# Optimization experiments

Measured on AMD Instinct MI355X. Metric: run time of the kernel, lower is better.

## Reference

```python
import jax, jax.numpy as jnp
import numpy as np

B = 32768      # rows
L = 512        # sequence_length
H = 1024       # inter_layer_size
E = 128        # encoding_size
K = 8          # number of (shifting_type, transformer_ID) combinations / decoders


def setup_inputs() -> dict:
    key = jax.random.key(0)
    ks = jax.random.split(key, 8)
    feats = jax.random.normal(ks[0], (B, L), jnp.float32)
    ids = jax.random.randint(ks[1], (B,), 0, K).astype(jnp.float32)
    x = jnp.concatenate([feats, ids[:, None]], axis=1)  # [B, L+1], last col = combination ID

    def init_w(k, shape, fan_in):
        return jax.random.normal(k, shape, jnp.float32) / np.float32(np.sqrt(fan_in))

    # shared encoder: Linear(L->H), Linear(H->E)  (weights stored [in, out])
    We1 = init_w(ks[2], (L, H), L); be1 = jnp.zeros((H,), jnp.float32)
    We2 = init_w(ks[3], (H, E), H); be2 = jnp.zeros((E,), jnp.float32)
    # per-ID decoders stacked along expert dim K: Linear(E->H), Linear(H->L)
    Wd1 = init_w(ks[4], (K, E, H), E); bd1 = jnp.zeros((K, H), jnp.float32)
    Wd2 = init_w(ks[5], (K, H, L), H); bd2 = jnp.zeros((K, L), jnp.float32)
    return dict(x=x, We1=We1, be1=be1, We2=We2, be2=be2,
                Wd1=Wd1, bd1=bd1, Wd2=Wd2, bd2=bd2)


def reference(x, We1, be1, We2, be2, Wd1, bd1, Wd2, bd2):
    seq_len = We1.shape[0]
    n_experts = Wd1.shape[0]
    ids = x[:, seq_len].astype(jnp.int32)          # routing column
    # torch code emits rows grouped by unique ID (torch.unique returns sorted ids);
    # jnp.argsort is stable, so within-group original order is preserved.
    order = jnp.argsort(ids)
    xs = x[order, :seq_len]                        # [B, L] grouped features
    ids_s = ids[order]                             # [B]

    # shared encoder MLP (LeakyReLU slope 0.01, torch default)
    h = jax.nn.leaky_relu(xs @ We1 + be1)          # [B, H]
    z = jax.nn.leaky_relu(h @ We2 + be2)           # [B, E]

    # dense expert dispatch: run every decoder, select per-row expert via one-hot
    hd = jax.nn.leaky_relu(jnp.einsum('be,keh->kbh', z, Wd1) + bd1[:, None, :])  # [K, B, H]
    y_all = jnp.einsum('kbh,khl->kbl', hd, Wd2) + bd2[:, None, :]                # [K, B, L]
    onehot = (ids_s[None, :] == jnp.arange(n_experts)[:, None]).astype(y_all.dtype)  # [K, B]
    return jnp.einsum('kb,kbl->bl', onehot, y_all)  # [B, L]
```

## Files before the change

### kernel.cpp

```cpp
#include <hip/hip_runtime.h>
#include <hip/hip_bf16.h>

#define B_ROWS 32768
#define L_DIM 512
#define H_DIM 1024
#define E_DIM 128
#define K_EXP 8
#define NBLK 128

typedef __bf16 bf16x8 __attribute__((ext_vector_type(8)));
typedef float f32x4 __attribute__((ext_vector_type(4)));

__device__ __forceinline__ void gload16(const void* src, void* dst) {
    __builtin_amdgcn_global_load_lds(
        (const __attribute__((address_space(1))) unsigned int*)src,
        (__attribute__((address_space(3))) unsigned int*)dst, 16, 0, 0);
}

__global__ void k_ids_hist(const float* __restrict__ x, int* __restrict__ ids,
                           int* __restrict__ hist) {
    __shared__ int lh[K_EXP];
    int t = threadIdx.x;
    if (t < K_EXP) lh[t] = 0;
    __syncthreads();
    int i = blockIdx.x * 256 + t;
    int id = (int)x[(size_t)i * (L_DIM + 1) + L_DIM];
    ids[i] = id;
    atomicAdd(&lh[id], 1);
    __syncthreads();
    if (t < K_EXP) hist[blockIdx.x * K_EXP + t] = lh[t];
}

__global__ void k_scan(const int* __restrict__ hist, int* __restrict__ base,
                       int* __restrict__ seg, int* __restrict__ tp) {
    __shared__ int c[K_EXP];
    __shared__ int sseg[K_EXP + 1];
    int k = threadIdx.x;
    if (k < K_EXP) {
        int run = 0;
        for (int b = 0; b < NBLK; ++b) {
            base[b * K_EXP + k] = run;
            run += hist[b * K_EXP + k];
        }
        c[k] = run;
    }
    __syncthreads();
    if (k == 0) {
        int s = 0, t2 = 0;
        for (int e = 0; e < K_EXP; ++e) {
            sseg[e] = s; seg[e] = s; tp[e] = t2;
            s += c[e]; t2 += (c[e] + 127) >> 7;
        }
        sseg[K_EXP] = s; seg[K_EXP] = s; tp[K_EXP] = t2;
    }
    __syncthreads();
    if (k < K_EXP) {
        int s0 = sseg[k];
        for (int b = 0; b < NBLK; ++b) base[b * K_EXP + k] += s0;
    }
}

__global__ void k_order(const int* __restrict__ ids, const int* __restrict__ base,
                        int* __restrict__ order) {
    __shared__ int sid[256];
    int t = threadIdx.x;
    int i = blockIdx.x * 256 + t;
    int my = ids[i];
    sid[t] = my;
    __syncthreads();
    int rank = 0;
    for (int j = 0; j < t; ++j) rank += (sid[j] == my) ? 1 : 0;
    order[base[blockIdx.x * K_EXP + my] + rank] = i;
}

__global__ void k_gather(const float* __restrict__ x, const int* __restrict__ order,
                         __hip_bfloat16* __restrict__ xs) {
    int idx = blockIdx.x * 256 + threadIdx.x;
    int p = idx >> 7;
    int c4 = (idx & 127) << 2;
    int src = order[p];
    const float* sp = x + (size_t)src * (L_DIM + 1) + c4;
    __hip_bfloat16 v[4];
    v[0] = __float2bfloat16(sp[0]);
    v[1] = __float2bfloat16(sp[1]);
    v[2] = __float2bfloat16(sp[2]);
    v[3] = __float2bfloat16(sp[3]);
    *(uint2*)(xs + (size_t)p * L_DIM + c4) = *(uint2*)v;
}

__global__ void k_transpose(const float* __restrict__ W, __hip_bfloat16* __restrict__ Wt,
                            int KDim, int NDim) {
    __shared__ float tile[32][33];
    int k0 = blockIdx.x << 5, n0 = blockIdx.y << 5;
    const float* Wb = W + (size_t)blockIdx.z * KDim * NDim;
    __hip_bfloat16* Wtb = Wt + (size_t)blockIdx.z * KDim * NDim;
    int tx = threadIdx.x & 31, ty = threadIdx.x >> 5;
    for (int i = ty; i < 32; i += 8)
        tile[i][tx] = Wb[(size_t)(k0 + i) * NDim + n0 + tx];
    __syncthreads();
    for (int i = ty; i < 32; i += 8)
        Wtb[(size_t)(n0 + i) * KDim + k0 + tx] = __float2bfloat16(tile[tx][i]);
}

template <int BM, int KD, int ND, bool GROUPED, bool LEAKY, bool OUT_BF16>
__launch_bounds__(256)
__global__ void gemm_u(const __hip_bfloat16* __restrict__ A,
                       const __hip_bfloat16* __restrict__ Bt,
                       const float* __restrict__ bias,
                       void* __restrict__ Cout,
                       const int* __restrict__ seg, const int* __restrict__ tp) {
    static_assert(!GROUPED || BM == 128, "grouped tiles are 128 rows");
    constexpr int NNT = ND / 128;
    constexpr int NMT = GROUPED ? (B_ROWS / 128 + K_EXP) : (B_ROWS / BM);
    constexpr int TOT = NMT * NNT;
    static_assert(TOT % 8 == 0, "XCD chunking needs TOT % 8 == 0");
    constexpr int ACH = BM * 32;
    constexpr int SLOT = ACH + 128 * 32;
    constexpr int NK = KD / 32;
    constexpr int VG = (BM == 128) ? 4 : 3;

    __shared__ __align__(16) __hip_bfloat16 smem[3 * SLOT];
    const int id = blockIdx.x;
    const int wg = (id & 7) * (TOT / 8) + (id >> 3);
    const int mt = wg / NNT, nt = wg % NNT;
    const int n0 = nt << 7;
    int m0, mEnd;
    const __hip_bfloat16* Bp = Bt;
    const float* bp = bias;
    if (GROUPED) {
        if (mt >= tp[K_EXP]) return;
        int e = 0;
        while (mt >= tp[e + 1]) ++e;
        m0 = seg[e] + ((mt - tp[e]) << 7);
        mEnd = seg[e + 1];
        Bp += (size_t)e * KD * ND;
        bp += (size_t)e * ND;
    } else {
        m0 = mt * BM;
        mEnd = m0 + BM;
    }
    const int t = threadIdx.x, w = t >> 6, l = t & 63;
    constexpr int FM = BM / 32;
    const int wm = w >> 1, wn = w & 1, g = l >> 4, li = l & 15;
    const int r0 = l >> 2, s0 = l & 3;

    f32x4 acc[FM][4];
#pragma unroll
    for (int i = 0; i < FM; ++i)
#pragma unroll
        for (int j = 0; j < 4; ++j) acc[i][j] = (f32x4){0.f, 0.f, 0.f, 0.f};

    auto stage = [&](int b, int kt) {
#pragma unroll
        for (int qi = 0; qi < BM / 64; ++qi) {
            int q = (BM / 64) * w + qi;
            int r = q * 16 + r0;
            int ksg = s0 ^ ((r >> 1) & 3);
            int rowg = m0 + r;
            if (GROUPED) rowg = min(rowg, B_ROWS - 1);
            gload16(A + (size_t)rowg * KD + kt * 32 + ksg * 8,
                    &smem[b * SLOT + q * 512]);
        }
#pragma unroll
        for (int qi = 0; qi < 2; ++qi) {
            int q = 2 * w + qi;
            int r = q * 16 + r0;
            int ksg = s0 ^ ((r >> 1) & 3);
            gload16(Bp + (size_t)(n0 + r) * KD + kt * 32 + ksg * 8,
                    &smem[b * SLOT + ACH + q * 512]);
        }
    };

    stage(0, 0);
    stage(1, 1);
    int b = 0;
    for (int kt = 0; kt < NK; ++kt) {
        if (kt == NK - 1)
            asm volatile("s_waitcnt vmcnt(0)\ns_barrier" ::: "memory");
        else if constexpr (VG == 4)
            asm volatile("s_waitcnt vmcnt(4)\ns_barrier" ::: "memory");
        else
            asm volatile("s_waitcnt vmcnt(3)\ns_barrier" ::: "memory");
        __builtin_amdgcn_sched_barrier(0);
        if (kt + 2 < NK) stage((b + 2 >= 3) ? b - 1 : b + 2, kt + 2);
        bf16x8 af[FM], bfr[4];
#pragma unroll
        for (int fm = 0; fm < FM; ++fm) {
            int rr = wm * (FM * 16) + fm * 16 + li;
            int ss = g ^ ((rr >> 1) & 3);
            af[fm] = *(const bf16x8*)&smem[b * SLOT + rr * 32 + ss * 8];
        }
#pragma unroll
        for (int fn = 0; fn < 4; ++fn) {
            int cc = wn * 64 + fn * 16 + li;
            int ss = g ^ ((cc >> 1) & 3);
            bfr[fn] = *(const bf16x8*)&smem[b * SLOT + ACH + cc * 32 + ss * 8];
        }
        __builtin_amdgcn_s_setprio(1);
#pragma unroll
        for (int fm = 0; fm < FM; ++fm)
#pragma unroll
            for (int fn = 0; fn < 4; ++fn)
                acc[fm][fn] = __builtin_amdgcn_mfma_f32_16x16x32_bf16(
                    af[fm], bfr[fn], acc[fm][fn], 0, 0, 0);
        __builtin_amdgcn_s_setprio(0);
        b = (b + 1 >= 3) ? 0 : b + 1;
    }

    float bv[4];
#pragma unroll
    for (int fn = 0; fn < 4; ++fn) bv[fn] = bp[n0 + wn * 64 + fn * 16 + li];
#pragma unroll
    for (int fm = 0; fm < FM; ++fm)
#pragma unroll
        for (int i = 0; i < 4; ++i) {
            int r = m0 + wm * (FM * 16) + fm * 16 + g * 4 + i;
            if (!GROUPED || r < mEnd) {
#pragma unroll
                for (int fn = 0; fn < 4; ++fn) {
                    float v = acc[fm][fn][i] + bv[fn];
                    if (LEAKY) v = v > 0.f ? v : 0.01f * v;
                    size_t off = (size_t)r * ND + n0 + wn * 64 + fn * 16 + li;
                    if (OUT_BF16)
                        ((__hip_bfloat16*)Cout)[off] = __float2bfloat16(v);
                    else
                        ((float*)Cout)[off] = v;
                }
            }
        }
}

extern "C" void kernel_launch(void* const* d_in, const int* in_sizes, int n_in,
                              void* d_out, int out_size, void* d_ws, size_t ws_size,
                              hipStream_t stream) {
    (void)in_sizes; (void)n_in; (void)out_size; (void)ws_size;
    const float* x   = (const float*)d_in[0];
    const float* We1 = (const float*)d_in[1];
    const float* be1 = (const float*)d_in[2];
    const float* We2 = (const float*)d_in[3];
    const float* be2 = (const float*)d_in[4];
    const float* Wd1 = (const float*)d_in[5];
    const float* bd1 = (const float*)d_in[6];
    const float* Wd2 = (const float*)d_in[7];
    const float* bd2 = (const float*)d_in[8];
    float* out = (float*)d_out;

    char* w = (char*)d_ws;
    auto alloc = [&](size_t bytes) {
        char* p = w;
        w += (bytes + 255) & ~(size_t)255;
        return p;
    };
    int* ids   = (int*)alloc((size_t)B_ROWS * 4);
    int* order = (int*)alloc((size_t)B_ROWS * 4);
    int* hist  = (int*)alloc((size_t)NBLK * K_EXP * 4);
    int* base  = (int*)alloc((size_t)NBLK * K_EXP * 4);
    int* seg   = (int*)alloc((K_EXP + 1) * 4);
    int* tp    = (int*)alloc((K_EXP + 1) * 4);
    __hip_bfloat16* xs   = (__hip_bfloat16*)alloc((size_t)B_ROWS * L_DIM * 2);
    __hip_bfloat16* hbuf = (__hip_bfloat16*)alloc((size_t)B_ROWS * H_DIM * 2);
    __hip_bfloat16* zbuf = (__hip_bfloat16*)alloc((size_t)B_ROWS * E_DIM * 2);
    __hip_bfloat16* Wt1  = (__hip_bfloat16*)alloc((size_t)L_DIM * H_DIM * 2);
    __hip_bfloat16* Wt2  = (__hip_bfloat16*)alloc((size_t)H_DIM * E_DIM * 2);
    __hip_bfloat16* Wd1t = (__hip_bfloat16*)alloc((size_t)K_EXP * E_DIM * H_DIM * 2);
    __hip_bfloat16* Wd2t = (__hip_bfloat16*)alloc((size_t)K_EXP * H_DIM * L_DIM * 2);

    k_ids_hist<<<NBLK, 256, 0, stream>>>(x, ids, hist);
    k_scan<<<1, 64, 0, stream>>>(hist, base, seg, tp);
    k_order<<<NBLK, 256, 0, stream>>>(ids, base, order);
    k_gather<<<(B_ROWS * (L_DIM / 4)) / 256, 256, 0, stream>>>(x, order, xs);

    k_transpose<<<dim3(L_DIM / 32, H_DIM / 32, 1), 256, 0, stream>>>(We1, Wt1, L_DIM, H_DIM);
    k_transpose<<<dim3(H_DIM / 32, E_DIM / 32, 1), 256, 0, stream>>>(We2, Wt2, H_DIM, E_DIM);
    k_transpose<<<dim3(E_DIM / 32, H_DIM / 32, K_EXP), 256, 0, stream>>>(Wd1, Wd1t, E_DIM, H_DIM);
    k_transpose<<<dim3(H_DIM / 32, L_DIM / 32, K_EXP), 256, 0, stream>>>(Wd2, Wd2t, H_DIM, L_DIM);

    gemm_u<128, L_DIM, H_DIM, false, true, true>
        <<<(B_ROWS / 128) * (H_DIM / 128), 256, 0, stream>>>(xs, Wt1, be1, hbuf, nullptr, nullptr);
    gemm_u<64, H_DIM, E_DIM, false, true, true>
        <<<(B_ROWS / 64) * (E_DIM / 128), 256, 0, stream>>>(hbuf, Wt2, be2, zbuf, nullptr, nullptr);
    gemm_u<128, E_DIM, H_DIM, true, true, true>
        <<<(B_ROWS / 128 + K_EXP) * (H_DIM / 128), 256, 0, stream>>>(zbuf, Wd1t, bd1, hbuf, seg, tp);
    gemm_u<128, H_DIM, L_DIM, true, false, false>
        <<<(B_ROWS / 128 + K_EXP) * (L_DIM / 128), 256, 0, stream>>>(hbuf, Wd2t, bd2, out, seg, tp);
}
```

Baseline: 208.6 us.

## Pad expert segments to 128-row tiles and use 128x256 GEMM tiles

Rows are now scattered into a padded layout where each expert segment starts on a 128-row boundary. That removes the per-row bounds checks and the min-clamping on A loads, and lets the padded buffer run the whole encoder and decoder chain. The first-layer and decoder GEMMs move to a wider 128x256 tile, with each wave computing 128x64 and launch bounds set for two blocks per CU. The final GEMM maps padded rows back to their sorted output positions. Padding adds up to 1024 extra rows of computation, and the larger per-wave accumulator raises register pressure.

```diff
diff --git a/kernel.cpp b/kernel.cpp
--- a/kernel.cpp
+++ b/kernel.cpp
@@ -7,6 +7,8 @@
 #define E_DIM 128
 #define K_EXP 8
 #define NBLK 128
+#define MAXT 264
+#define MAXB (MAXT * 128)
 
 typedef __bf16 bf16x8 __attribute__((ext_vector_type(8)));
 typedef float f32x4 __attribute__((ext_vector_type(4)));
@@ -16,6 +18,12 @@
         (const __attribute__((address_space(1))) unsigned int*)src,
         (__attribute__((address_space(3))) unsigned int*)dst, 16, 0, 0);
 }
+
+#define M_NT 0
+#define M_SEG 1
+#define M_SEGP 10
+#define M_CNT 19
+#define M_TEXP 27
 
 __global__ void k_ids_hist(const float* __restrict__ x, int* __restrict__ ids,
                            int* __restrict__ hist) {
@@ -32,9 +40,10 @@
 }
 
 __global__ void k_scan(const int* __restrict__ hist, int* __restrict__ base,
-                       int* __restrict__ seg, int* __restrict__ tp) {
+                       int* __restrict__ meta, int* __restrict__ order_pad) {
     __shared__ int c[K_EXP];
-    __shared__ int sseg[K_EXP + 1];
+    __shared__ int sp[K_EXP + 1];
+    __shared__ int scnt[K_EXP];
     int k = threadIdx.x;
     if (k < K_EXP) {
         int run = 0;
@@ -46,18 +55,36 @@
     }
     __syncthreads();
     if (k == 0) {
-        int s = 0, t2 = 0;
+        int s = 0, p = 0;
         for (int e = 0; e < K_EXP; ++e) {
-            sseg[e] = s; seg[e] = s; tp[e] = t2;
-            s += c[e]; t2 += (c[e] + 127) >> 7;
-        }
-        sseg[K_EXP] = s; seg[K_EXP] = s; tp[K_EXP] = t2;
+            meta[M_SEG + e] = s;
+            meta[M_SEGP + e] = p;
+            meta[M_CNT + e] = c[e];
+            sp[e] = p;
+            scnt[e] = c[e];
+            s += c[e];
+            p += ((c[e] + 127) >> 7) << 7;
+        }
+        meta[M_SEG + K_EXP] = s;
+        meta[M_SEGP + K_EXP] = p;
+        sp[K_EXP] = p;
+        int nT = p >> 7;
+        meta[M_NT] = nT;
+        for (int e = 0; e < K_EXP; ++e)
+            for (int t2 = sp[e] >> 7; t2 < sp[e + 1] >> 7; ++t2)
+                meta[M_TEXP + t2] = e;
+        for (int t2 = nT; t2 < MAXT; ++t2) meta[M_TEXP + t2] = 0;
     }
     __syncthreads();
     if (k < K_EXP) {
-        int s0 = sseg[k];
+        int s0 = sp[k];
         for (int b = 0; b < NBLK; ++b) base[b * K_EXP + k] += s0;
     }
+    for (int e = 0; e < K_EXP; ++e) {
+        int st = sp[e] + scnt[e], en = sp[e + 1];
+        for (int p2 = st + k; p2 < en; p2 += 64) order_pad[p2] = 0;
+    }
+    for (int p2 = sp[K_EXP] + k; p2 < MAXB; p2 += 64) order_pad[p2] = 0;
 }
 
 __global__ void k_order(const int* __restrict__ ids, const int* __restrict__ base,
@@ -102,72 +129,59 @@
         Wtb[(size_t)(n0 + i) * KDim + k0 + tx] = __float2bfloat16(tile[tx][i]);
 }
 
-template <int BM, int KD, int ND, bool GROUPED, bool LEAKY, bool OUT_BF16>
-__launch_bounds__(256)
-__global__ void gemm_u(const __hip_bfloat16* __restrict__ A,
+template <int KD, int ND, bool GROUPED, bool LEAKY, bool OUT_BF16, bool MAPROW>
+__launch_bounds__(256, 2)
+__global__ void gemm_w(const __hip_bfloat16* __restrict__ A,
                        const __hip_bfloat16* __restrict__ Bt,
                        const float* __restrict__ bias,
                        void* __restrict__ Cout,
-                       const int* __restrict__ seg, const int* __restrict__ tp) {
-    static_assert(!GROUPED || BM == 128, "grouped tiles are 128 rows");
-    constexpr int NNT = ND / 128;
-    constexpr int NMT = GROUPED ? (B_ROWS / 128 + K_EXP) : (B_ROWS / BM);
-    constexpr int TOT = NMT * NNT;
+                       const int* __restrict__ meta) {
+    constexpr int NNT = ND / 256;
+    constexpr int TOT = MAXT * NNT;
     static_assert(TOT % 8 == 0, "XCD chunking needs TOT % 8 == 0");
-    constexpr int ACH = BM * 32;
-    constexpr int SLOT = ACH + 128 * 32;
+    constexpr int ASZ = 128 * 32;
+    constexpr int SLOT = ASZ + 256 * 32;
     constexpr int NK = KD / 32;
-    constexpr int VG = (BM == 128) ? 4 : 3;
 
     __shared__ __align__(16) __hip_bfloat16 smem[3 * SLOT];
     const int id = blockIdx.x;
     const int wg = (id & 7) * (TOT / 8) + (id >> 3);
     const int mt = wg / NNT, nt = wg % NNT;
-    const int n0 = nt << 7;
-    int m0, mEnd;
+    const int m0 = mt << 7, n0 = nt << 8;
     const __hip_bfloat16* Bp = Bt;
     const float* bp = bias;
+    int e = 0;
     if (GROUPED) {
-        if (mt >= tp[K_EXP]) return;
-        int e = 0;
-        while (mt >= tp[e + 1]) ++e;
-        m0 = seg[e] + ((mt - tp[e]) << 7);
-        mEnd = seg[e + 1];
+        e = meta[M_TEXP + mt];
         Bp += (size_t)e * KD * ND;
         bp += (size_t)e * ND;
-    } else {
-        m0 = mt * BM;
-        mEnd = m0 + BM;
     }
     const int t = threadIdx.x, w = t >> 6, l = t & 63;
-    constexpr int FM = BM / 32;
-    const int wm = w >> 1, wn = w & 1, g = l >> 4, li = l & 15;
+    const int g = l >> 4, li = l & 15;
     const int r0 = l >> 2, s0 = l & 3;
 
-    f32x4 acc[FM][4];
-#pragma unroll
-    for (int i = 0; i < FM; ++i)
+    f32x4 acc[8][4];
+#pragma unroll
+    for (int i = 0; i < 8; ++i)
 #pragma unroll
         for (int j = 0; j < 4; ++j) acc[i][j] = (f32x4){0.f, 0.f, 0.f, 0.f};
 
     auto stage = [&](int b, int kt) {
-#pragma unroll
-        for (int qi = 0; qi < BM / 64; ++qi) {
-            int q = (BM / 64) * w + qi;
-            int r = q * 16 + r0;
-            int ksg = s0 ^ ((r >> 1) & 3);
-            int rowg = m0 + r;
-            if (GROUPED) rowg = min(rowg, B_ROWS - 1);
-            gload16(A + (size_t)rowg * KD + kt * 32 + ksg * 8,
-                    &smem[b * SLOT + q * 512]);
-        }
 #pragma unroll
         for (int qi = 0; qi < 2; ++qi) {
             int q = 2 * w + qi;
             int r = q * 16 + r0;
             int ksg = s0 ^ ((r >> 1) & 3);
+            gload16(A + (size_t)(m0 + r) * KD + kt * 32 + ksg * 8,
+                    &smem[b * SLOT + q * 512]);
+        }
+#pragma unroll
+        for (int qi = 0; qi < 4; ++qi) {
+            int q = 4 * w + qi;
+            int r = q * 16 + r0;
+            int ksg = s0 ^ ((r >> 1) & 3);
             gload16(Bp + (size_t)(n0 + r) * KD + kt * 32 + ksg * 8,
-                    &smem[b * SLOT + ACH + q * 512]);
+                    &smem[b * SLOT + ASZ + q * 512]);
         }
     };
 
@@ -177,28 +191,26 @@
     for (int kt = 0; kt < NK; ++kt) {
         if (kt == NK - 1)
             asm volatile("s_waitcnt vmcnt(0)\ns_barrier" ::: "memory");
-        else if constexpr (VG == 4)
-            asm volatile("s_waitcnt vmcnt(4)\ns_barrier" ::: "memory");
         else
-            asm volatile("s_waitcnt vmcnt(3)\ns_barrier" ::: "memory");
+            asm volatile("s_waitcnt vmcnt(6)\ns_barrier" ::: "memory");
         __builtin_amdgcn_sched_barrier(0);
         if (kt + 2 < NK) stage((b + 2 >= 3) ? b - 1 : b + 2, kt + 2);
-        bf16x8 af[FM], bfr[4];
-#pragma unroll
-        for (int fm = 0; fm < FM; ++fm) {
-            int rr = wm * (FM * 16) + fm * 16 + li;
+        bf16x8 af[8], bfr[4];
+#pragma unroll
+        for (int fm = 0; fm < 8; ++fm) {
+            int rr = fm * 16 + li;
             int ss = g ^ ((rr >> 1) & 3);
             af[fm] = *(const bf16x8*)&smem[b * SLOT + rr * 32 + ss * 8];
         }
 #pragma unroll
         for (int fn = 0; fn < 4; ++fn) {
-            int cc = wn * 64 + fn * 16 + li;
+            int cc = w * 64 + fn * 16 + li;
             int ss = g ^ ((cc >> 1) & 3);
-            bfr[fn] = *(const bf16x8*)&smem[b * SLOT + ACH + cc * 32 + ss * 8];
+            bfr[fn] = *(const bf16x8*)&smem[b * SLOT + ASZ + cc * 32 + ss * 8];
         }
         __builtin_amdgcn_s_setprio(1);
 #pragma unroll
-        for (int fm = 0; fm < FM; ++fm)
+        for (int fm = 0; fm < 8; ++fm)
 #pragma unroll
             for (int fn = 0; fn < 4; ++fn)
                 acc[fm][fn] = __builtin_amdgcn_mfma_f32_16x16x32_bf16(
@@ -209,23 +221,126 @@
 
     float bv[4];
 #pragma unroll
-    for (int fn = 0; fn < 4; ++fn) bv[fn] = bp[n0 + wn * 64 + fn * 16 + li];
-#pragma unroll
-    for (int fm = 0; fm < FM; ++fm)
+    for (int fn = 0; fn < 4; ++fn) bv[fn] = bp[n0 + w * 64 + fn * 16 + li];
+    int se = 0, sp2 = 0, ce = 0;
+    if (MAPROW) { se = meta[M_SEG + e]; sp2 = meta[M_SEGP + e]; ce = meta[M_CNT + e]; }
+#pragma unroll
+    for (int fm = 0; fm < 8; ++fm)
 #pragma unroll
         for (int i = 0; i < 4; ++i) {
-            int r = m0 + wm * (FM * 16) + fm * 16 + g * 4 + i;
-            if (!GROUPED || r < mEnd) {
-#pragma unroll
-                for (int fn = 0; fn < 4; ++fn) {
-                    float v = acc[fm][fn][i] + bv[fn];
-                    if (LEAKY) v = v > 0.f ? v : 0.01f * v;
-                    size_t off = (size_t)r * ND + n0 + wn * 64 + fn * 16 + li;
-                    if (OUT_BF16)
-                        ((__hip_bfloat16*)Cout)[off] = __float2bfloat16(v);
-                    else
-                        ((float*)Cout)[off] = v;
+            int rp = m0 + fm * 16 + g * 4 + i;
+#pragma unroll
+            for (int fn = 0; fn < 4; ++fn) {
+                float v = acc[fm][fn][i] + bv[fn];
+                if (LEAKY) v = v > 0.f ? v : 0.01f * v;
+                int col = n0 + w * 64 + fn * 16 + li;
+                if (MAPROW) {
+                    int local = rp - sp2;
+                    if (local < ce)
+                        ((float*)Cout)[(size_t)(se + local) * ND + col] = v;
+                } else if (OUT_BF16) {
+                    ((__hip_bfloat16*)Cout)[(size_t)rp * ND + col] = __float2bfloat16(v);
+                } else {
+                    ((float*)Cout)[(size_t)rp * ND + col] = v;
                 }
+            }
+        }
+}
+
+template <int KD, int ND, bool LEAKY>
+__launch_bounds__(256)
+__global__ void gemm_u64(const __hip_bfloat16* __restrict__ A,
+                         const __hip_bfloat16* __restrict__ Bt,
+                         const float* __restrict__ bias,
+                         __hip_bfloat16* __restrict__ Cout) {
+    constexpr int BM = 64;
+    constexpr int NNT = ND / 128;
+    constexpr int NMT = MAXB / BM;
+    constexpr int TOT = NMT * NNT;
+    static_assert(TOT % 8 == 0, "XCD chunking needs TOT % 8 == 0");
+    constexpr int ACH = BM * 32;
+    constexpr int SLOT = ACH + 128 * 32;
+    constexpr int NK = KD / 32;
+
+    __shared__ __align__(16) __hip_bfloat16 smem[3 * SLOT];
+    const int id = blockIdx.x;
+    const int wg = (id & 7) * (TOT / 8) + (id >> 3);
+    const int mt = wg / NNT, nt = wg % NNT;
+    const int n0 = nt << 7;
+    const int m0 = mt * BM;
+    const int t = threadIdx.x, w = t >> 6, l = t & 63;
+    const int wm = w >> 1, wn = w & 1, g = l >> 4, li = l & 15;
+    const int r0 = l >> 2, s0 = l & 3;
+
+    f32x4 acc[2][4];
+#pragma unroll
+    for (int i = 0; i < 2; ++i)
+#pragma unroll
+        for (int j = 0; j < 4; ++j) acc[i][j] = (f32x4){0.f, 0.f, 0.f, 0.f};
+
+    auto stage = [&](int b, int kt) {
+        {
+            int q = w, r = q * 16 + r0;
+            int ksg = s0 ^ ((r >> 1) & 3);
+            gload16(A + (size_t)(m0 + r) * KD + kt * 32 + ksg * 8,
+                    &smem[b * SLOT + q * 512]);
+        }
+#pragma unroll
+        for (int qi = 0; qi < 2; ++qi) {
+            int q = 2 * w + qi, r = q * 16 + r0;
+            int ksg = s0 ^ ((r >> 1) & 3);
+            gload16(Bt + (size_t)(n0 + r) * KD + kt * 32 + ksg * 8,
+                    &smem[b * SLOT + ACH + q * 512]);
+        }
+    };
+
+    stage(0, 0);
+    stage(1, 1);
+    int b = 0;
+    for (int kt = 0; kt < NK; ++kt) {
+        if (kt == NK - 1)
+            asm volatile("s_waitcnt vmcnt(0)\ns_barrier" ::: "memory");
+        else
+            asm volatile("s_waitcnt vmcnt(3)\ns_barrier" ::: "memory");
+        __builtin_amdgcn_sched_barrier(0);
+        if (kt + 2 < NK) stage((b + 2 >= 3) ? b - 1 : b + 2, kt + 2);
+        bf16x8 af[2], bfr[4];
+#pragma unroll
+        for (int fm = 0; fm < 2; ++fm) {
+            int rr = wm * 32 + fm * 16 + li;
+            int ss = g ^ ((rr >> 1) & 3);
+            af[fm] = *(const bf16x8*)&smem[b * SLOT + rr * 32 + ss * 8];
+        }
+#pragma unroll
+        for (int fn = 0; fn < 4; ++fn) {
+            int cc = wn * 64 + fn * 16 + li;
+            int ss = g ^ ((cc >> 1) & 3);
+            bfr[fn] = *(const bf16x8*)&smem[b * SLOT + ACH + cc * 32 + ss * 8];
+        }
+        __builtin_amdgcn_s_setprio(1);
+#pragma unroll
+        for (int fm = 0; fm < 2; ++fm)
+#pragma unroll
+            for (int fn = 0; fn < 4; ++fn)
+                acc[fm][fn] = __builtin_amdgcn_mfma_f32_16x16x32_bf16(
+                    af[fm], bfr[fn], acc[fm][fn], 0, 0, 0);
+        __builtin_amdgcn_s_setprio(0);
+        b = (b + 1 >= 3) ? 0 : b + 1;
+    }
+
+    float bv[4];
+#pragma unroll
+    for (int fn = 0; fn < 4; ++fn) bv[fn] = bias[n0 + wn * 64 + fn * 16 + li];
+#pragma unroll
+    for (int fm = 0; fm < 2; ++fm)
+#pragma unroll
+        for (int i = 0; i < 4; ++i) {
+            int r = m0 + wm * 32 + fm * 16 + g * 4 + i;
+#pragma unroll
+            for (int fn = 0; fn < 4; ++fn) {
+                float v = acc[fm][fn][i] + bv[fn];
+                if (LEAKY) v = v > 0.f ? v : 0.01f * v;
+                Cout[(size_t)r * ND + n0 + wn * 64 + fn * 16 + li] = __float2bfloat16(v);
             }
         }
 }
@@ -251,36 +366,35 @@
         w += (bytes + 255) & ~(size_t)255;
         return p;
     };
-    int* ids   = (int*)alloc((size_t)B_ROWS * 4);
-    int* order = (int*)alloc((size_t)B_ROWS * 4);
-    int* hist  = (int*)alloc((size_t)NBLK * K_EXP * 4);
-    int* base  = (int*)alloc((size_t)NBLK * K_EXP * 4);
-    int* seg   = (int*)alloc((K_EXP + 1) * 4);
-    int* tp    = (int*)alloc((K_EXP + 1) * 4);
-    __hip_bfloat16* xs   = (__hip_bfloat16*)alloc((size_t)B_ROWS * L_DIM * 2);
-    __hip_bfloat16* hbuf = (__hip_bfloat16*)alloc((size_t)B_ROWS * H_DIM * 2);
-    __hip_bfloat16* zbuf = (__hip_bfloat16*)alloc((size_t)B_ROWS * E_DIM * 2);
+    int* ids       = (int*)alloc((size_t)B_ROWS * 4);
+    int* order_pad = (int*)alloc((size_t)MAXB * 4);
+    int* hist      = (int*)alloc((size_t)NBLK * K_EXP * 4);
+    int* base      = (int*)alloc((size_t)NBLK * K_EXP * 4);
+    int* meta      = (int*)alloc((size_t)(M_TEXP + MAXT) * 4);
+    __hip_bfloat16* xs   = (__hip_bfloat16*)alloc((size_t)MAXB * L_DIM * 2);
+    __hip_bfloat16* hbuf = (__hip_bfloat16*)alloc((size_t)MAXB * H_DIM * 2);
+    __hip_bfloat16* zbuf = (__hip_bfloat16*)alloc((size_t)MAXB * E_DIM * 2);
     __hip_bfloat16* Wt1  = (__hip_bfloat16*)alloc((size_t)L_DIM * H_DIM * 2);
     __hip_bfloat16* Wt2  = (__hip_bfloat16*)alloc((size_t)H_DIM * E_DIM * 2);
     __hip_bfloat16* Wd1t = (__hip_bfloat16*)alloc((size_t)K_EXP * E_DIM * H_DIM * 2);
     __hip_bfloat16* Wd2t = (__hip_bfloat16*)alloc((size_t)K_EXP * H_DIM * L_DIM * 2);
 
     k_ids_hist<<<NBLK, 256, 0, stream>>>(x, ids, hist);
-    k_scan<<<1, 64, 0, stream>>>(hist, base, seg, tp);
-    k_order<<<NBLK, 256, 0, stream>>>(ids, base, order);
-    k_gather<<<(B_ROWS * (L_DIM / 4)) / 256, 256, 0, stream>>>(x, order, xs);
+    k_scan<<<1, 64, 0, stream>>>(hist, base, meta, order_pad);
+    k_order<<<NBLK, 256, 0, stream>>>(ids, base, order_pad);
+    k_gather<<<(MAXB * (L_DIM / 4)) / 256, 256, 0, stream>>>(x, order_pad, xs);
 
     k_transpose<<<dim3(L_DIM / 32, H_DIM / 32, 1), 256, 0, stream>>>(We1, Wt1, L_DIM, H_DIM);
     k_transpose<<<dim3(H_DIM / 32, E_DIM / 32, 1), 256, 0, stream>>>(We2, Wt2, H_DIM, E_DIM);
     k_transpose<<<dim3(E_DIM / 32, H_DIM / 32, K_EXP), 256, 0, stream>>>(Wd1, Wd1t, E_DIM, H_DIM);
     k_transpose<<<dim3(H_DIM / 32, L_DIM / 32, K_EXP), 256, 0, stream>>>(Wd2, Wd2t, H_DIM, L_DIM);
 
-    gemm_u<128, L_DIM, H_DIM, false, true, true>
-        <<<(B_ROWS / 128) * (H_DIM / 128), 256, 0, stream>>>(xs, Wt1, be1, hbuf, nullptr, nullptr);
-    gemm_u<64, H_DIM, E_DIM, false, true, true>
-        <<<(B_ROWS / 64) * (E_DIM / 128), 256, 0, stream>>>(hbuf, Wt2, be2, zbuf, nullptr, nullptr);
-    gemm_u<128, E_DIM, H_DIM, true, true, true>
-        <<<(B_ROWS / 128 + K_EXP) * (H_DIM / 128), 256, 0, stream>>>(zbuf, Wd1t, bd1, hbuf, seg, tp);
-    gemm_u<128, H_DIM, L_DIM, true, false, false>
-        <<<(B_ROWS / 128 + K_EXP) * (L_DIM / 128), 256, 0, stream>>>(hbuf, Wd2t, bd2, out, seg, tp);
-}
+    gemm_w<L_DIM, H_DIM, false, true, true, false>
+        <<<MAXT * (H_DIM / 256), 256, 0, stream>>>(xs, Wt1, be1, hbuf, meta);
+    gemm_u64<H_DIM, E_DIM, true>
+        <<<(MAXB / 64) * (E_DIM / 128), 256, 0, stream>>>(hbuf, Wt2, be2, zbuf);
+    gemm_w<E_DIM, H_DIM, true, true, true, false>
+        <<<MAXT * (H_DIM / 256), 256, 0, stream>>>(zbuf, Wd1t, bd1, hbuf, meta);
+    gemm_w<H_DIM, L_DIM, true, false, false, true>
+        <<<MAXT * (L_DIM / 256), 256, 0, stream>>>(hbuf, Wd2t, bd2, out, meta);
+}
```

Result: slower. 229.8 us (+10.2%).
